# Performance work log

Measured on AMD Instinct MI355X. Metric: run time of the kernel, lower is better.

Reference implementation:

```python
import jax, jax.numpy as jnp
import numpy as np

N, C, E, K = 50000, 128, 640000, 40  # nodes, feat dim, edges, classes
EPS = 1e-5


def setup_inputs() -> dict:
    key = jax.random.key(0)
    ks = jax.random.split(key, 8)
    s = 1.0 / np.sqrt(C)
    return {
        "x": jax.random.normal(ks[0], (N, C), jnp.float32),
        "edge_index": jax.random.randint(ks[1], (2, E), 0, N, dtype=jnp.int32),
        "W_conv": jax.random.normal(ks[2], (C, C), jnp.float32) * s,
        "b_conv": jnp.zeros((C,), jnp.float32),
        "gamma": jnp.ones((C,), jnp.float32),
        "beta": jnp.zeros((C,), jnp.float32),
        "W_fc": jax.random.normal(ks[3], (C, K), jnp.float32) * s,
        "b_fc": jnp.zeros((K,), jnp.float32),
    }


def reference(x, edge_index, W_conv, b_conv, gamma, beta, W_fc, b_fc):
    n = x.shape[0]
    loops = jnp.arange(n, dtype=edge_index.dtype)
    src = jnp.concatenate([edge_index[0], loops])  # add self-loops (PyG default)
    dst = jnp.concatenate([edge_index[1], loops])
    # symmetric normalization: deg^{-1/2}[src] * deg^{-1/2}[dst]
    deg = jax.ops.segment_sum(jnp.ones_like(dst, jnp.float32), dst, num_segments=n)
    dinv = jax.lax.rsqrt(jnp.maximum(deg, 1.0))  # deg >= 1 with self-loops
    norm = dinv[src] * dinv[dst]  # [E+N]
    h = x @ W_conv  # [N, C] transform before propagate (GCNConv)
    agg = jax.ops.segment_sum(h[src] * norm[:, None], dst, num_segments=n) + b_conv
    a = jax.nn.relu(agg) * x  # dropout = identity (eval mode); elementwise mul with residual
    mu = jnp.mean(a, axis=-1, keepdims=True)
    var = jnp.mean((a - mu) ** 2, axis=-1, keepdims=True)
    ln = (a - mu) * jax.lax.rsqrt(var + EPS) * gamma + beta
    return (ln + x) @ W_fc + b_fc
```

## Files before the change

kernel.cpp:

```cpp
#include <hip/hip_runtime.h>

#define C_DIM 128
#define EPS 1e-5f
#define CSTRIDE 16

typedef __attribute__((ext_vector_type(8))) short short8;
typedef __attribute__((ext_vector_type(4))) float f32x4;

__device__ __forceinline__ unsigned bf16rn(float f) {
    unsigned u = __float_as_uint(f);
    return (u + 0x7fffu + ((u >> 16) & 1u)) >> 16;
}
__device__ __forceinline__ unsigned pack_bf16(float lo, float hi) {
    return bf16rn(lo) | (bf16rn(hi) << 16);
}
__device__ __forceinline__ float blo(unsigned u) { return __uint_as_float(u << 16); }
__device__ __forceinline__ float bhi(unsigned u) { return __uint_as_float(u & 0xffff0000u); }

__global__ void prep0(const float* __restrict__ W, const float* __restrict__ Wfc,
                      unsigned short* __restrict__ WhT, unsigned short* __restrict__ WlT,
                      unsigned short* __restrict__ WT,
                      float4* __restrict__ cz, int czn) {
    int gid = blockIdx.x * blockDim.x + threadIdx.x;
    int stride = gridDim.x * blockDim.x;
    for (int t = gid; t < 128 * 128; t += stride) {
        int c = t >> 7, k = t & 127;
        float v = W[k * 128 + c];
        unsigned hi = bf16rn(v);
        float fh = __uint_as_float(hi << 16);
        WhT[c * 128 + k] = (unsigned short)hi;
        WlT[c * 128 + k] = (unsigned short)bf16rn(v - fh);
    }
    for (int t = gid; t < 48 * 128; t += stride) {
        int nc = t >> 7, k = t & 127;
        WT[nc * 128 + k] = (unsigned short)((nc < 40) ? bf16rn(Wfc[k * 40 + nc]) : 0u);
    }
    float4 z = make_float4(0.f, 0.f, 0.f, 0.f);
    for (int t = gid; t < czn; t += stride) cz[t] = z;
}

__global__ __launch_bounds__(256, 4) void fat(const float* __restrict__ x,
                                              const unsigned short* __restrict__ WhT,
                                              const unsigned short* __restrict__ WlT,
                                              unsigned short* __restrict__ hbs,
                                              const int* __restrict__ esrc,
                                              const int* __restrict__ edst,
                                              int* __restrict__ cntA,
                                              int* __restrict__ cntB,
                                              unsigned short* __restrict__ bsrcu,
                                              int n, int e, int g1) {
    int b = blockIdx.x;
    int t = threadIdx.x;

    if (b < g1) {
        int r0 = b * 128;
        int wid = t >> 6, lane = t & 63;
        int mrow = lane & 15, quad = lane >> 4;
        int rb = r0 + wid * 32;

        f32x4 acc[2][8];
#pragma unroll
        for (int m = 0; m < 2; m++)
#pragma unroll
            for (int nn = 0; nn < 8; nn++) acc[m][nn] = (f32x4){0.f, 0.f, 0.f, 0.f};

#pragma unroll
        for (int ks = 0; ks < 4; ks++) {
            short8 Ah[2], Al[2];
#pragma unroll
            for (int m = 0; m < 2; m++) {
                int r = rb + m * 16 + mrow;
                if (r >= n) r = n - 1;
                const float* xp = &x[(long)r * C_DIM + ks * 32 + quad * 8];
                float4 va = *(const float4*)xp;
                float4 vb = *(const float4*)(xp + 4);
                float xv[8] = {va.x, va.y, va.z, va.w, vb.x, vb.y, vb.z, vb.w};
#pragma unroll
                for (int e8 = 0; e8 < 8; e8++) {
                    unsigned hi = bf16rn(xv[e8]);
                    Ah[m][e8] = (short)hi;
                    Al[m][e8] = (short)bf16rn(xv[e8] - __uint_as_float(hi << 16));
                }
            }
#pragma unroll
            for (int nn = 0; nn < 8; nn++) {
                int wof = (nn * 16 + mrow) * 128 + ks * 32 + quad * 8;
                short8 Bh = *(const short8*)&WhT[wof];
                short8 Bl = *(const short8*)&WlT[wof];
#pragma unroll
                for (int m = 0; m < 2; m++) {
                    acc[m][nn] = __builtin_amdgcn_mfma_f32_16x16x32_bf16(Ah[m], Bh, acc[m][nn], 0, 0, 0);
                    acc[m][nn] = __builtin_amdgcn_mfma_f32_16x16x32_bf16(Al[m], Bh, acc[m][nn], 0, 0, 0);
                    acc[m][nn] = __builtin_amdgcn_mfma_f32_16x16x32_bf16(Ah[m], Bl, acc[m][nn], 0, 0, 0);
                }
            }
        }
#pragma unroll
        for (int m = 0; m < 2; m++)
#pragma unroll
            for (int nn = 0; nn < 8; nn++) {
                int c = nn * 16 + mrow;
#pragma unroll
                for (int reg = 0; reg < 4; reg++) {
                    int r = rb + m * 16 + quad * 4 + reg;
                    if (r < n) hbs[(long)r * 128 + c] = (unsigned short)bf16rn(acc[m][nn][reg]);
                }
            }
    } else {
        int sb = b - g1;
        int q = (e + 3) >> 2;
        int i0 = sb * 256 + t;
        int i1 = i0 + q, i2 = i0 + 2 * q, i3 = i0 + 3 * q;
        bool v0 = i0 < e, v1 = i1 < e, v2 = i2 < e, v3 = i3 < e;
        int d0 = v0 ? edst[i0] : 0, s0 = v0 ? esrc[i0] : 0;
        int d1 = v1 ? edst[i1] : 0, s1 = v1 ? esrc[i1] : 0;
        int d2 = v2 ? edst[i2] : 0, s2 = v2 ? esrc[i2] : 0;
        int d3 = v3 ? edst[i3] : 0, s3 = v3 ? esrc[i3] : 0;
        int p0 = v0 ? atomicAdd(&cntA[(long)d0 * CSTRIDE], 1) : 64;
        int p1 = v1 ? atomicAdd(&cntA[(long)d1 * CSTRIDE], 1) : 64;
        int p2 = v2 ? atomicAdd(&cntB[(long)d2 * CSTRIDE], 1) : 64;
        int p3 = v3 ? atomicAdd(&cntB[(long)d3 * CSTRIDE], 1) : 64;
        if (p0 < 64) bsrcu[(long)d0 * 64 + p0] = (unsigned short)s0;
        if (p1 < 64) bsrcu[(long)d1 * 64 + p1] = (unsigned short)s1;
        if (p2 < 64) bsrcu[(long)d2 * 64 + 63 - p2] = (unsigned short)s2;
        if (p3 < 64) bsrcu[(long)d3 * 64 + 63 - p3] = (unsigned short)s3;
    }
}

__global__ __launch_bounds__(256) void d0(const unsigned* __restrict__ hb,
                                          const int* __restrict__ cntA,
                                          const int* __restrict__ cntB,
                                          unsigned* __restrict__ hb2, int n) {
    int gid = blockIdx.x * 256 + threadIdx.x;
    if (gid >= n * 16) return;
    int row = gid >> 4;
    float di = rsqrtf((float)(cntA[(long)row * CSTRIDE] + cntB[(long)row * CSTRIDE]) + 1.0f);
    uint4 u = ((const uint4*)hb)[gid];
    uint4 o;
    o.x = pack_bf16(di * blo(u.x), di * bhi(u.x));
    o.y = pack_bf16(di * blo(u.y), di * bhi(u.y));
    o.z = pack_bf16(di * blo(u.z), di * bhi(u.z));
    o.w = pack_bf16(di * blo(u.w), di * bhi(u.w));
    ((uint4*)hb2)[gid] = o;
}

__global__ __launch_bounds__(256) void aggregate(const unsigned* __restrict__ hb2,
                                                 const float* __restrict__ x,
                                                 const int* __restrict__ cntA,
                                                 const int* __restrict__ cntB,
                                                 const unsigned short* __restrict__ bsrcu,
                                                 const float* __restrict__ bconv,
                                                 const float* __restrict__ gamma,
                                                 const float* __restrict__ beta,
                                                 unsigned* __restrict__ zb, int n) {
    int wid = (blockIdx.x * blockDim.x + threadIdx.x) >> 6;
    if (wid >= n) return;
    int lane = threadIdx.x & 63;
    int sub = lane & 15, grp = lane >> 4;
    int i = wid;

    uint4 us = *(const uint4*)(hb2 + (long)i * 64 + sub * 4);
    float4 xa = *(const float4*)&x[(long)i * C_DIM + sub * 8];
    float4 xb = *(const float4*)&x[(long)i * C_DIM + sub * 8 + 4];
    int sraw = (int)bsrcu[(long)i * 64 + lane];

    int dA = cntA[(long)i * CSTRIDE], dB = cntB[(long)i * CSTRIDE];
    float di = rsqrtf((float)(dA + dB) + 1.0f);
    if (dA > 64) dA = 64;
    if (dB > 64 - dA) dB = 64 - dA;
    int tot = dA + dB;
    int shift = 64 - tot;

    int s_all = ((lane < dA) | (lane >= 64 - dB)) ? sraw : 0;

    float wself = (grp == 0) ? 1.f : 0.f;
    float acc[8];
    acc[0] = wself * blo(us.x); acc[1] = wself * bhi(us.x);
    acc[2] = wself * blo(us.y); acc[3] = wself * bhi(us.y);
    acc[4] = wself * blo(us.z); acc[5] = wself * bhi(us.z);
    acc[6] = wself * blo(us.w); acc[7] = wself * bhi(us.w);

    int nIt = (tot + 15) >> 4;
    for (int it = 0; it < nIt; ++it) {
        int tb = grp + it * 16;
        int ss[4];
        float ww[4];
#pragma unroll
        for (int qq = 0; qq < 4; qq++) {
            int tq = tb + qq * 4;
            int slq = ((tq < dA) ? tq : tq + shift) & 63;
            int sq = __shfl(s_all, slq);
            float wq = 1.f;
            if (tq >= tot) { wq = 0.f; sq = i; }
            ss[qq] = sq;
            ww[qq] = wq;
        }
        uint4 u[4];
#pragma unroll
        for (int qq = 0; qq < 4; qq++) u[qq] = *(const uint4*)(hb2 + (long)ss[qq] * 64 + sub * 4);
#pragma unroll
        for (int qq = 0; qq < 4; qq++) {
            float w = ww[qq];
            acc[0] += w * blo(u[qq].x); acc[1] += w * bhi(u[qq].x);
            acc[2] += w * blo(u[qq].y); acc[3] += w * bhi(u[qq].y);
            acc[4] += w * blo(u[qq].z); acc[5] += w * bhi(u[qq].z);
            acc[6] += w * blo(u[qq].w); acc[7] += w * bhi(u[qq].w);
        }
    }

#pragma unroll
    for (int j = 0; j < 8; j++) {
        acc[j] += __shfl_xor(acc[j], 16);
        acc[j] += __shfl_xor(acc[j], 32);
    }

    float4 bca = *(const float4*)&bconv[sub * 8];
    float4 bcb = *(const float4*)&bconv[sub * 8 + 4];
    float a[8], xv[8];
    xv[0] = xa.x; xv[1] = xa.y; xv[2] = xa.z; xv[3] = xa.w;
    xv[4] = xb.x; xv[5] = xb.y; xv[6] = xb.z; xv[7] = xb.w;
    float bc[8] = {bca.x, bca.y, bca.z, bca.w, bcb.x, bcb.y, bcb.z, bcb.w};
#pragma unroll
    for (int j = 0; j < 8; j++) a[j] = fmaxf(acc[j] * di + bc[j], 0.f) * xv[j];

    float s = a[0] + a[1] + a[2] + a[3] + a[4] + a[5] + a[6] + a[7];
#pragma unroll
    for (int off = 1; off < 16; off <<= 1) s += __shfl_xor(s, off);
    float mu = s * (1.0f / 128.0f);
    float d[8], v = 0.f;
#pragma unroll
    for (int j = 0; j < 8; j++) { d[j] = a[j] - mu; v += d[j] * d[j]; }
#pragma unroll
    for (int off = 1; off < 16; off <<= 1) v += __shfl_xor(v, off);
    float inv = rsqrtf(v * (1.0f / 128.0f) + EPS);

    if (grp == 0) {
        float4 ga = *(const float4*)&gamma[sub * 8];
        float4 gb = *(const float4*)&gamma[sub * 8 + 4];
        float4 ba = *(const float4*)&beta[sub * 8];
        float4 bb = *(const float4*)&beta[sub * 8 + 4];
        float g[8] = {ga.x, ga.y, ga.z, ga.w, gb.x, gb.y, gb.z, gb.w};
        float be[8] = {ba.x, ba.y, ba.z, ba.w, bb.x, bb.y, bb.z, bb.w};
        float o[8];
#pragma unroll
        for (int j = 0; j < 8; j++) o[j] = d[j] * inv * g[j] + be[j] + xv[j];
        uint4 p;
        p.x = pack_bf16(o[0], o[1]);
        p.y = pack_bf16(o[2], o[3]);
        p.z = pack_bf16(o[4], o[5]);
        p.w = pack_bf16(o[6], o[7]);
        *(uint4*)(zb + (long)i * 64 + sub * 4) = p;
    }
}

__global__ __launch_bounds__(256) void gemm2(const unsigned short* __restrict__ zb,
                                             const unsigned short* __restrict__ WT,
                                             const float* __restrict__ bfc,
                                             float* __restrict__ out, int n) {
    int t = threadIdx.x;
    int w = t >> 6, lane = t & 63;
    int r0 = blockIdx.x * 64 + w * 16;
    if (r0 >= n) return;
    int mrow = lane & 15;
    int quad = lane >> 4;
    f32x4 acc[3];
#pragma unroll
    for (int nt = 0; nt < 3; nt++) acc[nt] = (f32x4){0.f, 0.f, 0.f, 0.f};
#pragma unroll
    for (int ks = 0; ks < 4; ks++) {
        int r = r0 + mrow;
        if (r >= n) r = n - 1;
        short8 A = *(const short8*)&zb[(long)r * 128 + ks * 32 + quad * 8];
        short8 B[3];
#pragma unroll
        for (int nt = 0; nt < 3; nt++)
            B[nt] = *(const short8*)&WT[(nt * 16 + mrow) * 128 + ks * 32 + quad * 8];
#pragma unroll
        for (int nt = 0; nt < 3; nt++)
            acc[nt] = __builtin_amdgcn_mfma_f32_16x16x32_bf16(A, B[nt], acc[nt], 0, 0, 0);
    }
#pragma unroll
    for (int nt = 0; nt < 3; nt++) {
        int c = nt * 16 + mrow;
        if (c < 40) {
            float bias = bfc[c];
#pragma unroll
            for (int reg = 0; reg < 4; reg++) {
                int r = r0 + quad * 4 + reg;
                if (r < n) out[(long)r * 40 + c] = acc[nt][reg] + bias;
            }
        }
    }
}

extern "C" void kernel_launch(void* const* d_in, const int* in_sizes, int n_in,
                              void* d_out, int out_size, void* d_ws, size_t ws_size,
                              hipStream_t stream) {
    const float* x     = (const float*)d_in[0];
    const int*   ei    = (const int*)d_in[1];
    const float* Wc    = (const float*)d_in[2];
    const float* bc    = (const float*)d_in[3];
    const float* gamma = (const float*)d_in[4];
    const float* beta  = (const float*)d_in[5];
    const float* Wfc   = (const float*)d_in[6];
    const float* bfc   = (const float*)d_in[7];
    float* out = (float*)d_out;

    int N = in_sizes[0] / C_DIM;
    int E = in_sizes[1] / 2;
    const int* esrc = ei;
    const int* edst = ei + E;

    char* p = (char*)d_ws;
    auto carve = [&](size_t bytes) {
        void* q = (void*)p;
        p += (bytes + 255) & ~(size_t)255;
        return q;
    };
    unsigned* hb        = (unsigned*)carve((size_t)N * 64 * 4);
    unsigned* hb2       = (unsigned*)carve((size_t)N * 64 * 4);
    unsigned short* WT  = (unsigned short*)carve(48 * 128 * 2);
    unsigned short* WhT = (unsigned short*)carve(128 * 128 * 2);
    unsigned short* WlT = (unsigned short*)carve(128 * 128 * 2);
    int* cntA           = (int*)carve((size_t)N * CSTRIDE * 4);
    int* cntB           = (int*)carve((size_t)N * CSTRIDE * 4);
    unsigned short* bsrcu = (unsigned short*)carve((size_t)N * 64 * 2);

    unsigned* zb = hb;

    int czn = (N * CSTRIDE * 2) / 4;
    prep0<<<256, 256, 0, stream>>>(Wc, Wfc, WhT, WlT, WT, (float4*)cntA, czn);

    int g1 = (N + 127) / 128;
    int nscat = (((E + 3) >> 2) + 255) / 256;
    fat<<<g1 + nscat, 256, 0, stream>>>(x, WhT, WlT, (unsigned short*)hb, esrc, edst,
                                        cntA, cntB, bsrcu, N, E, g1);

    d0<<<(N * 16 + 255) / 256, 256, 0, stream>>>(hb, cntA, cntB, hb2, N);

    aggregate<<<((size_t)N * 64 + 255) / 256, 256, 0, stream>>>(
        hb2, x, cntA, cntB, bsrcu, bc, gamma, beta, zb, N);

    gemm2<<<(N + 63) / 64, 256, 0, stream>>>((const unsigned short*)zb, WT, bfc, out, N);
}
```

Baseline: 185.0 us.

## Replace atomic bucket scatter with two-level counting sort into CSR

Replaces the per-destination global atomic counters and fixed 64-slot buckets with a deterministic counting sort. Edges are histogrammed into 64-node bins per block, the histograms are scanned, the edges are scattered into bin-contiguous records, and each bin is then sorted into a CSR row layout. The dinv scaling is folded into the CSR kernel. This aims to remove contended global atomics and strided counter traffic, and it also drops the 64-neighbor cap. In exchange it adds more kernel launches, a scan stage and an extra pass over the edge records.

```diff
diff --git a/kernel.cpp b/kernel.cpp
--- a/kernel.cpp
+++ b/kernel.cpp
@@ -2,7 +2,8 @@
 
 #define C_DIM 128
 #define EPS 1e-5f
-#define CSTRIDE 16
+#define NBIN 784
+#define SBLK 2048
 
 typedef __attribute__((ext_vector_type(8))) short short8;
 typedef __attribute__((ext_vector_type(4))) float f32x4;
@@ -17,43 +18,156 @@
 __device__ __forceinline__ float blo(unsigned u) { return __uint_as_float(u << 16); }
 __device__ __forceinline__ float bhi(unsigned u) { return __uint_as_float(u & 0xffff0000u); }
 
-__global__ void prep0(const float* __restrict__ W, const float* __restrict__ Wfc,
-                      unsigned short* __restrict__ WhT, unsigned short* __restrict__ WlT,
-                      unsigned short* __restrict__ WT,
-                      float4* __restrict__ cz, int czn) {
-    int gid = blockIdx.x * blockDim.x + threadIdx.x;
-    int stride = gridDim.x * blockDim.x;
-    for (int t = gid; t < 128 * 128; t += stride) {
-        int c = t >> 7, k = t & 127;
-        float v = W[k * 128 + c];
-        unsigned hi = bf16rn(v);
-        float fh = __uint_as_float(hi << 16);
-        WhT[c * 128 + k] = (unsigned short)hi;
-        WlT[c * 128 + k] = (unsigned short)bf16rn(v - fh);
-    }
-    for (int t = gid; t < 48 * 128; t += stride) {
-        int nc = t >> 7, k = t & 127;
-        WT[nc * 128 + k] = (unsigned short)((nc < 40) ? bf16rn(Wfc[k * 40 + nc]) : 0u);
-    }
-    float4 z = make_float4(0.f, 0.f, 0.f, 0.f);
-    for (int t = gid; t < czn; t += stride) cz[t] = z;
-}
-
-__global__ __launch_bounds__(256, 4) void fat(const float* __restrict__ x,
-                                              const unsigned short* __restrict__ WhT,
-                                              const unsigned short* __restrict__ WlT,
-                                              unsigned short* __restrict__ hbs,
-                                              const int* __restrict__ esrc,
+__device__ __forceinline__ void wave_scan_excl_lds(unsigned* buf, int lane) {
+    const int CH = (NBIN + 63) / 64;
+    unsigned v[CH];
+    unsigned s = 0;
+    int c0 = lane * CH;
+#pragma unroll
+    for (int k = 0; k < CH; k++) {
+        int idx = c0 + k;
+        v[k] = (idx < NBIN) ? buf[idx] : 0u;
+        s += v[k];
+    }
+    unsigned inc = s;
+#pragma unroll
+    for (int off = 1; off < 64; off <<= 1) {
+        unsigned tmp = __shfl_up(inc, off);
+        if (lane >= off) inc += tmp;
+    }
+    unsigned run = inc - s;
+#pragma unroll
+    for (int k = 0; k < CH; k++) {
+        int idx = c0 + k;
+        if (idx < NBIN) { buf[idx] = run; run += v[k]; }
+    }
+}
+
+__global__ __launch_bounds__(256) void k_hist(const float* __restrict__ W,
+                                              const float* __restrict__ Wfc,
+                                              unsigned short* __restrict__ WhT,
+                                              unsigned short* __restrict__ WlT,
+                                              unsigned short* __restrict__ WT,
                                               const int* __restrict__ edst,
-                                              int* __restrict__ cntA,
-                                              int* __restrict__ cntB,
-                                              unsigned short* __restrict__ bsrcu,
-                                              int n, int e, int g1) {
-    int b = blockIdx.x;
-    int t = threadIdx.x;
-
-    if (b < g1) {
-        int r0 = b * 128;
+                                              unsigned* __restrict__ H, int e, int ns) {
+    __shared__ unsigned lh[NBIN];
+    int b = blockIdx.x, t = threadIdx.x;
+    if (b < ns) {
+        for (int k = t; k < NBIN; k += 256) lh[k] = 0u;
+        __syncthreads();
+        int e0 = b * SBLK;
+        int lim = e - e0; if (lim > SBLK) lim = SBLK;
+        for (int k = t; k < lim; k += 256) atomicAdd(&lh[edst[e0 + k] >> 6], 1u);
+        __syncthreads();
+        for (int k = t; k < NBIN; k += 256) H[(size_t)b * NBIN + k] = lh[k];
+    } else {
+        int gid = (b - ns) * 256 + t;
+        int stride = ((int)gridDim.x - ns) * 256;
+        for (int i = gid; i < 128 * 128; i += stride) {
+            int c = i >> 7, k = i & 127;
+            float v = W[k * 128 + c];
+            unsigned hi = bf16rn(v);
+            WhT[c * 128 + k] = (unsigned short)hi;
+            WlT[c * 128 + k] = (unsigned short)bf16rn(v - __uint_as_float(hi << 16));
+        }
+        for (int i = gid; i < 48 * 128; i += stride) {
+            int nc = i >> 7, k = i & 127;
+            WT[nc * 128 + k] = (unsigned short)((nc < 40) ? bf16rn(Wfc[k * 40 + nc]) : 0u);
+        }
+    }
+}
+
+__global__ __launch_bounds__(256) void k_scan(unsigned* __restrict__ H,
+                                              unsigned* __restrict__ tot, int ns) {
+    int bin = blockIdx.x * 4 + (threadIdx.x >> 6);
+    int lane = threadIdx.x & 63;
+    if (bin >= NBIN) return;
+    unsigned run = 0;
+    for (int base = 0; base < ns; base += 64) {
+        int idx = base + lane;
+        unsigned v = (idx < ns) ? H[(size_t)idx * NBIN + bin] : 0u;
+        unsigned inc = v;
+#pragma unroll
+        for (int off = 1; off < 64; off <<= 1) {
+            unsigned tmp = __shfl_up(inc, off);
+            if (lane >= off) inc += tmp;
+        }
+        if (idx < ns) H[(size_t)idx * NBIN + bin] = run + inc - v;
+        run += __shfl(inc, 63);
+    }
+    if (lane == 0) tot[bin] = run;
+}
+
+__global__ void k_binscan(const unsigned* __restrict__ tot, unsigned* __restrict__ bstart) {
+    int lane = threadIdx.x;
+    const int CH = (NBIN + 63) / 64;
+    unsigned v[CH];
+    unsigned s = 0;
+    int c0 = lane * CH;
+#pragma unroll
+    for (int k = 0; k < CH; k++) {
+        int idx = c0 + k;
+        v[k] = (idx < NBIN) ? tot[idx] : 0u;
+        s += v[k];
+    }
+    unsigned inc = s;
+#pragma unroll
+    for (int off = 1; off < 64; off <<= 1) {
+        unsigned tmp = __shfl_up(inc, off);
+        if (lane >= off) inc += tmp;
+    }
+    unsigned run = inc - s;
+#pragma unroll
+    for (int k = 0; k < CH; k++) {
+        int idx = c0 + k;
+        if (idx < NBIN) { bstart[idx] = run; run += v[k]; }
+    }
+    if (lane == 63) bstart[NBIN] = run;
+}
+
+__global__ __launch_bounds__(256, 4) void k_sort(const float* __restrict__ x,
+                                                 const unsigned short* __restrict__ WhT,
+                                                 const unsigned short* __restrict__ WlT,
+                                                 unsigned short* __restrict__ hbs,
+                                                 const int* __restrict__ esrc,
+                                                 const int* __restrict__ edst,
+                                                 const unsigned* __restrict__ H,
+                                                 const unsigned* __restrict__ bstart,
+                                                 unsigned* __restrict__ recs,
+                                                 int n, int e, int ns) {
+    __shared__ unsigned bufA[NBIN];
+    __shared__ unsigned bufB[NBIN];
+    __shared__ unsigned bufC[NBIN];
+    __shared__ unsigned sbuf[SBLK];
+    int b = blockIdx.x, t = threadIdx.x;
+
+    if (b < ns) {
+        int e0 = b * SBLK;
+        int myE = e - e0; if (myE > SBLK) myE = SBLK;
+        for (int k = t; k < NBIN; k += 256) { bufC[k] = 0u; bufA[k] = 0u; }
+        __syncthreads();
+        for (int k = t; k < myE; k += 256) atomicAdd(&bufC[edst[e0 + k] >> 6], 1u);
+        for (int bin = t; bin < NBIN; bin += 256)
+            bufB[bin] = bstart[bin] + H[(size_t)b * NBIN + bin];
+        __syncthreads();
+        if (t < 64) wave_scan_excl_lds(bufC, t);
+        __syncthreads();
+        for (int k = t; k < myE; k += 256) {
+            int d = edst[e0 + k];
+            int s = esrc[e0 + k];
+            int bin = d >> 6;
+            unsigned lr = atomicAdd(&bufA[bin], 1u);
+            sbuf[bufC[bin] + lr] =
+                ((unsigned)bin << 22) | ((unsigned)(d & 63) << 16) | (unsigned)s;
+        }
+        __syncthreads();
+        for (int j = t; j < myE; j += 256) {
+            unsigned rec = sbuf[j];
+            unsigned bin = rec >> 22;
+            recs[bufB[bin] + (unsigned)j - bufC[bin]] = rec;
+        }
+    } else {
+        int r0 = (b - ns) * 128;
         int wid = t >> 6, lane = t & 63;
         int mrow = lane & 15, quad = lane >> 4;
         int rb = r0 + wid * 32;
@@ -106,49 +220,69 @@
                     if (r < n) hbs[(long)r * 128 + c] = (unsigned short)bf16rn(acc[m][nn][reg]);
                 }
             }
-    } else {
-        int sb = b - g1;
-        int q = (e + 3) >> 2;
-        int i0 = sb * 256 + t;
-        int i1 = i0 + q, i2 = i0 + 2 * q, i3 = i0 + 3 * q;
-        bool v0 = i0 < e, v1 = i1 < e, v2 = i2 < e, v3 = i3 < e;
-        int d0 = v0 ? edst[i0] : 0, s0 = v0 ? esrc[i0] : 0;
-        int d1 = v1 ? edst[i1] : 0, s1 = v1 ? esrc[i1] : 0;
-        int d2 = v2 ? edst[i2] : 0, s2 = v2 ? esrc[i2] : 0;
-        int d3 = v3 ? edst[i3] : 0, s3 = v3 ? esrc[i3] : 0;
-        int p0 = v0 ? atomicAdd(&cntA[(long)d0 * CSTRIDE], 1) : 64;
-        int p1 = v1 ? atomicAdd(&cntA[(long)d1 * CSTRIDE], 1) : 64;
-        int p2 = v2 ? atomicAdd(&cntB[(long)d2 * CSTRIDE], 1) : 64;
-        int p3 = v3 ? atomicAdd(&cntB[(long)d3 * CSTRIDE], 1) : 64;
-        if (p0 < 64) bsrcu[(long)d0 * 64 + p0] = (unsigned short)s0;
-        if (p1 < 64) bsrcu[(long)d1 * 64 + p1] = (unsigned short)s1;
-        if (p2 < 64) bsrcu[(long)d2 * 64 + 63 - p2] = (unsigned short)s2;
-        if (p3 < 64) bsrcu[(long)d3 * 64 + 63 - p3] = (unsigned short)s3;
-    }
-}
-
-__global__ __launch_bounds__(256) void d0(const unsigned* __restrict__ hb,
-                                          const int* __restrict__ cntA,
-                                          const int* __restrict__ cntB,
-                                          unsigned* __restrict__ hb2, int n) {
-    int gid = blockIdx.x * 256 + threadIdx.x;
-    if (gid >= n * 16) return;
-    int row = gid >> 4;
-    float di = rsqrtf((float)(cntA[(long)row * CSTRIDE] + cntB[(long)row * CSTRIDE]) + 1.0f);
-    uint4 u = ((const uint4*)hb)[gid];
-    uint4 o;
-    o.x = pack_bf16(di * blo(u.x), di * bhi(u.x));
-    o.y = pack_bf16(di * blo(u.y), di * bhi(u.y));
-    o.z = pack_bf16(di * blo(u.z), di * bhi(u.z));
-    o.w = pack_bf16(di * blo(u.w), di * bhi(u.w));
-    ((uint4*)hb2)[gid] = o;
+    }
+}
+
+__global__ __launch_bounds__(256) void k_csr(const unsigned* __restrict__ recs,
+                                             const unsigned* __restrict__ bstart,
+                                             const unsigned* __restrict__ hb,
+                                             unsigned* __restrict__ hb2,
+                                             unsigned short* __restrict__ csr,
+                                             unsigned* __restrict__ rowptr, int n) {
+    __shared__ unsigned nh[64], nstart[64], cur[64];
+    __shared__ float dinvl[64];
+    __shared__ unsigned short sl[4096];
+    int bin = blockIdx.x, t = threadIdx.x;
+    unsigned s0 = bstart[bin];
+    unsigned cn = bstart[bin + 1] - s0;
+    if (t < 64) { nh[t] = 0u; cur[t] = 0u; }
+    __syncthreads();
+    for (unsigned k = t; k < cn; k += 256) atomicAdd(&nh[(recs[s0 + k] >> 16) & 63u], 1u);
+    __syncthreads();
+    if (t < 64) {
+        unsigned v = nh[t];
+        unsigned inc = v;
+#pragma unroll
+        for (int off = 1; off < 64; off <<= 1) {
+            unsigned tmp = __shfl_up(inc, off);
+            if (t >= off) inc += tmp;
+        }
+        unsigned excl = inc - v;
+        nstart[t] = excl;
+        rowptr[bin * 64 + t] = s0 + excl;
+        dinvl[t] = rsqrtf((float)v + 1.0f);
+    }
+    __syncthreads();
+    for (unsigned k = t; k < cn; k += 256) {
+        unsigned rec = recs[s0 + k];
+        unsigned nd = (rec >> 16) & 63u;
+        unsigned r = atomicAdd(&cur[nd], 1u);
+        unsigned idx = nstart[nd] + r;
+        if (idx < 4096) sl[idx] = (unsigned short)(rec & 0xFFFFu);
+        else csr[s0 + idx] = (unsigned short)(rec & 0xFFFFu);
+    }
+    __syncthreads();
+    for (unsigned k = t; k < cn && k < 4096; k += 256) csr[s0 + k] = sl[k];
+    for (int idx = t; idx < 1024; idx += 256) {
+        int row = idx >> 4;
+        int node = bin * 64 + row;
+        if (node < n) {
+            float di = dinvl[row];
+            uint4 u = ((const uint4*)hb)[(size_t)node * 16 + (idx & 15)];
+            uint4 o;
+            o.x = pack_bf16(di * blo(u.x), di * bhi(u.x));
+            o.y = pack_bf16(di * blo(u.y), di * bhi(u.y));
+            o.z = pack_bf16(di * blo(u.z), di * bhi(u.z));
+            o.w = pack_bf16(di * blo(u.w), di * bhi(u.w));
+            ((uint4*)hb2)[(size_t)node * 16 + (idx & 15)] = o;
+        }
+    }
 }
 
 __global__ __launch_bounds__(256) void aggregate(const unsigned* __restrict__ hb2,
                                                  const float* __restrict__ x,
-                                                 const int* __restrict__ cntA,
-                                                 const int* __restrict__ cntB,
-                                                 const unsigned short* __restrict__ bsrcu,
+                                                 const unsigned short* __restrict__ csr,
+                                                 const unsigned* __restrict__ rowptr,
                                                  const float* __restrict__ bconv,
                                                  const float* __restrict__ gamma,
                                                  const float* __restrict__ beta,
@@ -159,19 +293,15 @@
     int sub = lane & 15, grp = lane >> 4;
     int i = wid;
 
+    unsigned rs = rowptr[i];
+    unsigned re = rowptr[i + 1];
+    int deg = (int)(re - rs);
+    float di = rsqrtf((float)deg + 1.0f);
+
     uint4 us = *(const uint4*)(hb2 + (long)i * 64 + sub * 4);
     float4 xa = *(const float4*)&x[(long)i * C_DIM + sub * 8];
     float4 xb = *(const float4*)&x[(long)i * C_DIM + sub * 8 + 4];
-    int sraw = (int)bsrcu[(long)i * 64 + lane];
-
-    int dA = cntA[(long)i * CSTRIDE], dB = cntB[(long)i * CSTRIDE];
-    float di = rsqrtf((float)(dA + dB) + 1.0f);
-    if (dA > 64) dA = 64;
-    if (dB > 64 - dA) dB = 64 - dA;
-    int tot = dA + dB;
-    int shift = 64 - tot;
-
-    int s_all = ((lane < dA) | (lane >= 64 - dB)) ? sraw : 0;
+    int s_all = (int)csr[rs + lane];
 
     float wself = (grp == 0) ? 1.f : 0.f;
     float acc[8];
@@ -180,18 +310,19 @@
     acc[4] = wself * blo(us.z); acc[5] = wself * bhi(us.z);
     acc[6] = wself * blo(us.w); acc[7] = wself * bhi(us.w);
 
-    int nIt = (tot + 15) >> 4;
+    int nIt = (deg + 15) >> 4;
     for (int it = 0; it < nIt; ++it) {
-        int tb = grp + it * 16;
         int ss[4];
         float ww[4];
 #pragma unroll
         for (int qq = 0; qq < 4; qq++) {
-            int tq = tb + qq * 4;
-            int slq = ((tq < dA) ? tq : tq + shift) & 63;
-            int sq = __shfl(s_all, slq);
+            int base = it * 16 + qq * 4;
+            int tq = base + grp;
+            int sq;
+            if (base >= 64) sq = (int)csr[rs + tq];
+            else sq = __shfl(s_all, tq);
             float wq = 1.f;
-            if (tq >= tot) { wq = 0.f; sq = i; }
+            if (tq >= deg) { wq = 0.f; sq = i; }
             ss[qq] = sq;
             ww[qq] = wq;
         }
@@ -310,6 +441,8 @@
     int E = in_sizes[1] / 2;
     const int* esrc = ei;
     const int* edst = ei + E;
+    int ns = (E + SBLK - 1) / SBLK;
+    int g1 = (N + 127) / 128;
 
     char* p = (char*)d_ws;
     auto carve = [&](size_t bytes) {
@@ -317,29 +450,27 @@
         p += (bytes + 255) & ~(size_t)255;
         return q;
     };
-    unsigned* hb        = (unsigned*)carve((size_t)N * 64 * 4);
-    unsigned* hb2       = (unsigned*)carve((size_t)N * 64 * 4);
-    unsigned short* WT  = (unsigned short*)carve(48 * 128 * 2);
-    unsigned short* WhT = (unsigned short*)carve(128 * 128 * 2);
-    unsigned short* WlT = (unsigned short*)carve(128 * 128 * 2);
-    int* cntA           = (int*)carve((size_t)N * CSTRIDE * 4);
-    int* cntB           = (int*)carve((size_t)N * CSTRIDE * 4);
-    unsigned short* bsrcu = (unsigned short*)carve((size_t)N * 64 * 2);
+    unsigned* hb         = (unsigned*)carve((size_t)N * 64 * 4);
+    unsigned* hb2        = (unsigned*)carve((size_t)N * 64 * 4);
+    unsigned short* WT   = (unsigned short*)carve(48 * 128 * 2);
+    unsigned short* WhT  = (unsigned short*)carve(128 * 128 * 2);
+    unsigned short* WlT  = (unsigned short*)carve(128 * 128 * 2);
+    unsigned* H          = (unsigned*)carve((size_t)ns * NBIN * 4);
+    unsigned* tot        = (unsigned*)carve((size_t)NBIN * 4);
+    unsigned* bstart     = (unsigned*)carve((size_t)(NBIN + 1) * 4);
+    unsigned* recs       = (unsigned*)carve((size_t)E * 4);
+    unsigned* rowptr     = (unsigned*)carve((size_t)(NBIN * 64 + 1) * 4);
+    unsigned short* csr  = (unsigned short*)carve((size_t)E * 2 + 256);
 
     unsigned* zb = hb;
 
-    int czn = (N * CSTRIDE * 2) / 4;
-    prep0<<<256, 256, 0, stream>>>(Wc, Wfc, WhT, WlT, WT, (float4*)cntA, czn);
-
-    int g1 = (N + 127) / 128;
-    int nscat = (((E + 3) >> 2) + 255) / 256;
-    fat<<<g1 + nscat, 256, 0, stream>>>(x, WhT, WlT, (unsigned short*)hb, esrc, edst,
-                                        cntA, cntB, bsrcu, N, E, g1);
-
-    d0<<<(N * 16 + 255) / 256, 256, 0, stream>>>(hb, cntA, cntB, hb2, N);
-
+    k_hist<<<ns + 64, 256, 0, stream>>>(Wc, Wfc, WhT, WlT, WT, edst, H, E, ns);
+    k_scan<<<NBIN / 4, 256, 0, stream>>>(H, tot, ns);
+    k_binscan<<<1, 64, 0, stream>>>(tot, bstart);
+    k_sort<<<ns + g1, 256, 0, stream>>>(x, WhT, WlT, (unsigned short*)hb, esrc, edst,
+                                        H, bstart, recs, N, E, ns);
+    k_csr<<<NBIN, 256, 0, stream>>>(recs, bstart, hb, hb2, csr, rowptr, N);
     aggregate<<<((size_t)N * 64 + 255) / 256, 256, 0, stream>>>(
-        hb2, x, cntA, cntB, bsrcu, bc, gamma, beta, zb, N);
-
+        hb2, x, csr, rowptr, bc, gamma, beta, zb, N);
     gemm2<<<(N + 63) / 64, 256, 0, stream>>>((const unsigned short*)zb, WT, bfc, out, N);
 }
```

Measured after the change: 171.7 us. 7.2% less time.
